# Optimization experiments

Hardware: AMD Instinct MI355X
Metric: run time of the kernel (lower is better)

The kernel has to match this reference:

```python
import jax, jax.numpy as jnp
import numpy as np

B, S, H = 32, 64, 512
ATT = 128


def _window_index_tables(seq_len):
    # Enumerate all contiguous windows of size 2..S, same set (order-independent
    # for the softmax-weighted sum) as the torch double loop.
    starts, ends = [], []
    for w in range(2, seq_len + 1):
        for s in range(0, seq_len - w + 1):
            starts.append(s)
            ends.append(s + w)
    starts = np.asarray(starts, np.int32)
    ends = np.asarray(ends, np.int32)
    widths = ends - starts
    ks = np.floor(np.log2(widths)).astype(np.int32)  # sparse-table level per window
    e2 = ends - (1 << ks)                            # second gather position
    return starts, e2, ks


def setup_inputs() -> dict:
    key = jax.random.key(0)
    k0, k1, k2, k3, k4 = jax.random.split(key, 5)
    return {
        "lstm_out": jax.random.normal(k0, (B, S, H), dtype=jnp.float32),
        "W1": jax.random.normal(k1, (H, ATT), dtype=jnp.float32) * 0.05,
        "b1": jax.random.normal(k2, (ATT,), dtype=jnp.float32) * 0.05,
        "W2": jax.random.normal(k3, (ATT, 1), dtype=jnp.float32) * 0.05,
        "b2": jax.random.normal(k4, (1,), dtype=jnp.float32) * 0.05,
    }


def reference(lstm_out, W1, b1, W2, b2):
    b, s, h = lstm_out.shape
    # Sparse table: M[k][:, i] = max over lstm_out[:, i : i+2^k] (clipped to s).
    n_levels = int(np.floor(np.log2(s))) + 1
    tables = [lstm_out]
    for k in range(1, n_levels):
        half = 1 << (k - 1)
        prev = tables[-1]
        shifted = jnp.concatenate(
            [prev[:, half:], jnp.full((b, half, h), -jnp.inf, prev.dtype)], axis=1)
        tables.append(jnp.maximum(prev, shifted))
    Mstack = jnp.stack(tables)  # [K, B, S, H]

    starts, e2, ks = _window_index_tables(s)
    # Range max of each window = max of two overlapping power-of-two blocks.
    pooled = jnp.maximum(Mstack[ks, :, starts], Mstack[ks, :, e2])  # [n_win, B, H]
    pooled = jnp.transpose(pooled, (1, 0, 2))  # [B, n_win, H]

    hid = jax.nn.relu(jnp.einsum("bnh,ha->bna", pooled, W1) + b1)
    scores = jnp.einsum("bna,ao->bno", hid, W2) + b2  # [B, n_win, 1]
    attn = jax.nn.softmax(scores, axis=1)
    return jnp.sum(attn * pooled, axis=1)  # [B, H]
```

## Files before the change

### kernel.cpp

```cpp
#include <hip/hip_runtime.h>
#include <stdint.h>

typedef unsigned short u16;
typedef unsigned int u32;

#define B_    32
#define S_    64
#define H_    512
#define ATT_  128
#define NWIN  2016
#define NLEV  7

typedef __bf16 bf16x8 __attribute__((ext_vector_type(8)));
typedef float  f32x4  __attribute__((ext_vector_type(4)));

__device__ __forceinline__ float bf2f(u16 u) {
  union { u32 i; float f; } v; v.i = ((u32)u) << 16; return v.f;
}
__device__ __forceinline__ u16 f2bf(float f) {
  union { float f; u32 i; } v; v.f = f;
  u32 i = v.i;
  i += 0x7fffu + ((i >> 16) & 1u);
  return (u16)(i >> 16);
}
__device__ __forceinline__ u32 bfmax2(u32 a, u32 b) {
  u16 a0 = (u16)(a & 0xffffu), a1 = (u16)(a >> 16);
  u16 b0 = (u16)(b & 0xffffu), b1 = (u16)(b >> 16);
  u16 m0 = (bf2f(a0) >= bf2f(b0)) ? a0 : b0;
  u16 m1 = (bf2f(a1) >= bf2f(b1)) ? a1 : b1;
  return (u32)m0 | ((u32)m1 << 16);
}
__device__ __forceinline__ uint4 bfmax8(uint4 a, uint4 b) {
  uint4 m;
  m.x = bfmax2(a.x, b.x); m.y = bfmax2(a.y, b.y);
  m.z = bfmax2(a.z, b.z); m.w = bfmax2(a.w, b.w);
  return m;
}

__launch_bounds__(256)
__global__ void k0_init(const float* __restrict__ W1, u16* __restrict__ w1t,
                        u16* __restrict__ widx) {
  int tid = threadIdx.x;
  if (blockIdx.x == 0) {
    for (int n = tid; n < NWIN; n += 256) {
      int w = 2, rem = n;
      while (rem >= 65 - w) { rem -= 65 - w; ++w; }
      int s = rem;
      int k = 31 - __clz(w);
      int e2 = s + w - (1 << k);
      widx[n] = (u16)(s | (e2 << 6) | (k << 12));
    }
  }
  int gid = blockIdx.x * 256 + tid;
  for (int idx = gid; idx < H_ * ATT_; idx += 64 * 256) {
    int n = idx >> 9, kq = idx & 511;
    w1t[idx] = f2bf(W1[kq * ATT_ + n]);
  }
}

__launch_bounds__(256)
__global__ void k1_table(const float* __restrict__ lstm, u16* __restrict__ table) {
  int hc = blockIdx.x, b = blockIdx.y, tid = threadIdx.x;
  __shared__ u16 bufA[64 * 64], bufB[64 * 64];
  const float* src = lstm + (size_t)b * S_ * H_ + hc * 64;
  u16* tb = table + (size_t)b * NLEV * S_ * H_ + hc * 64;
  for (int t = tid; t < 64 * 16; t += 256) {
    int r = t >> 4, c4 = t & 15;
    float4 f = *reinterpret_cast<const float4*>(src + r * H_ + c4 * 4);
    ushort4 u;
    u.x = f2bf(f.x); u.y = f2bf(f.y); u.z = f2bf(f.z); u.w = f2bf(f.w);
    *reinterpret_cast<ushort4*>(&bufA[r * 64 + c4 * 4]) = u;
    *reinterpret_cast<ushort4*>(tb + r * H_ + c4 * 4) = u;
  }
  u16* pa = bufA; u16* pb = bufB;
  for (int k = 1; k < NLEV; ++k) {
    __syncthreads();
    int half = 1 << (k - 1);
    u16* dst_g = tb + k * S_ * H_;
    for (int t = tid; t < 64 * 16; t += 256) {
      int r = t >> 4, c4 = t & 15;
      int r2 = r + half; if (r2 > 63) r2 = 63;
      uint2 a  = *reinterpret_cast<const uint2*>(&pa[r  * 64 + c4 * 4]);
      uint2 bq = *reinterpret_cast<const uint2*>(&pa[r2 * 64 + c4 * 4]);
      uint2 m; m.x = bfmax2(a.x, bq.x); m.y = bfmax2(a.y, bq.y);
      *reinterpret_cast<uint2*>(&pb[r * 64 + c4 * 4]) = m;
      *reinterpret_cast<uint2*>(dst_g + r * H_ + c4 * 4) = m;
    }
    u16* tmp = pa; pa = pb; pb = tmp;
  }
}

__launch_bounds__(256)
__global__ void k2_scores(const u16* __restrict__ table, const u16* __restrict__ w1t,
                          const float* __restrict__ b1, const float* __restrict__ w2,
                          const u16* __restrict__ widx, float* __restrict__ scores) {
  const int b = blockIdx.y, mt = blockIdx.x;
  __shared__ u16 As[96 * 72];
  __shared__ u16 Bs[128 * 72];
  __shared__ u16 widx_l[96];
  __shared__ float b1s[128], w2s[128], sc[96];
  int tid = threadIdx.x;
  if (tid < 96) { widx_l[tid] = widx[mt * 96 + tid]; sc[tid] = 0.f; }
  if (tid < 128) { b1s[tid] = b1[tid]; w2s[tid] = w2[tid]; }
  __syncthreads();

  const u16* tb = table + (size_t)b * NLEV * S_ * H_;
  int wid = tid >> 6, lane = tid & 63;
  int wm = wid & 1, wn = wid >> 1;
  int lrow = lane & 15, quad = lane >> 4;

  f32x4 acc[3][4];
#pragma unroll
  for (int i = 0; i < 3; ++i)
#pragma unroll
    for (int j = 0; j < 4; ++j) acc[i][j] = (f32x4){0.f, 0.f, 0.f, 0.f};

  for (int kk = 0; kk < H_; kk += 64) {
    for (int t = tid; t < 768; t += 256) {
      int r = t >> 3, c = t & 7;
      int pk = widx_l[r];
      int s = pk & 63, e2 = (pk >> 6) & 63, lv = pk >> 12;
      uint4 va = *reinterpret_cast<const uint4*>(tb + (lv * S_ + s) * H_ + kk + c * 8);
      uint4 vb = *reinterpret_cast<const uint4*>(tb + (lv * S_ + e2) * H_ + kk + c * 8);
      uint4 vm = bfmax8(va, vb);
      *reinterpret_cast<uint4*>(&As[r * 72 + c * 8]) = vm;
    }
    for (int t = tid; t < 1024; t += 256) {
      int n = t >> 3, c = t & 7;
      uint4 v = *reinterpret_cast<const uint4*>(w1t + n * H_ + kk + c * 8);
      *reinterpret_cast<uint4*>(&Bs[n * 72 + c * 8]) = v;
    }
    __syncthreads();
#pragma unroll
    for (int ks = 0; ks < 64; ks += 32) {
      bf16x8 af[3], bfr[4];
#pragma unroll
      for (int i = 0; i < 3; ++i)
        af[i] = *reinterpret_cast<const bf16x8*>(&As[(wm * 48 + i * 16 + lrow) * 72 + ks + quad * 8]);
#pragma unroll
      for (int j = 0; j < 4; ++j)
        bfr[j] = *reinterpret_cast<const bf16x8*>(&Bs[(wn * 64 + j * 16 + lrow) * 72 + ks + quad * 8]);
#pragma unroll
      for (int i = 0; i < 3; ++i)
#pragma unroll
        for (int j = 0; j < 4; ++j)
          acc[i][j] = __builtin_amdgcn_mfma_f32_16x16x32_bf16(af[i], bfr[j], acc[i][j], 0, 0, 0);
    }
    __syncthreads();
  }

#pragma unroll
  for (int i = 0; i < 3; ++i) {
#pragma unroll
    for (int r = 0; r < 4; ++r) {
      float p = 0.f;
#pragma unroll
      for (int j = 0; j < 4; ++j) {
        int n = wn * 64 + j * 16 + lrow;
        float v = acc[i][j][r] + b1s[n];
        p += (v > 0.f ? v : 0.f) * w2s[n];
      }
      p += __shfl_xor(p, 1, 16);
      p += __shfl_xor(p, 2, 16);
      p += __shfl_xor(p, 4, 16);
      p += __shfl_xor(p, 8, 16);
      if (lrow == 0) atomicAdd(&sc[wm * 48 + i * 16 + quad * 4 + r], p);
    }
  }
  __syncthreads();
  if (tid < 96) scores[b * NWIN + mt * 96 + tid] = sc[tid];
}

__launch_bounds__(256)
__global__ void k3_softmax(const float* __restrict__ scores, float* __restrict__ attn) {
  int b = blockIdx.x, tid = threadIdx.x;
  __shared__ float red[256];
  float mx = -1e30f;
  for (int n = tid; n < NWIN; n += 256) mx = fmaxf(mx, scores[b * NWIN + n]);
  red[tid] = mx; __syncthreads();
  for (int s = 128; s > 0; s >>= 1) {
    if (tid < s) red[tid] = fmaxf(red[tid], red[tid + s]);
    __syncthreads();
  }
  mx = red[0]; __syncthreads();
  float sum = 0.f;
  for (int n = tid; n < NWIN; n += 256) {
    float e = __expf(scores[b * NWIN + n] - mx);
    attn[b * NWIN + n] = e;
    sum += e;
  }
  red[tid] = sum; __syncthreads();
  for (int s = 128; s > 0; s >>= 1) {
    if (tid < s) red[tid] += red[tid + s];
    __syncthreads();
  }
  float inv = 1.f / red[0];
  __syncthreads();
  for (int n = tid; n < NWIN; n += 256) attn[b * NWIN + n] *= inv;
}

__launch_bounds__(256)
__global__ void k4_out(const u16* __restrict__ table, const float* __restrict__ attn,
                       const u16* __restrict__ widx, float* __restrict__ out) {
  int hc = blockIdx.x, b = blockIdx.y, tid = threadIdx.x;
  __shared__ u16 Tl[6 * 64 * 32];
  __shared__ float attn_l[NWIN];
  __shared__ u16 widx_l[NWIN];
  __shared__ float red[8][32];
  const u16* tb = table + (size_t)b * NLEV * S_ * H_ + S_ * H_;
  int h0 = hc * 32;
  for (int t = tid; t < 6 * 64 * 4; t += 256) {
    int row = t >> 2, c = t & 3;
    uint4 v = *reinterpret_cast<const uint4*>(tb + row * H_ + h0 + c * 8);
    *reinterpret_cast<uint4*>(&Tl[row * 32 + c * 8]) = v;
  }
  for (int n = tid; n < NWIN; n += 256) {
    attn_l[n] = attn[b * NWIN + n];
    widx_l[n] = widx[n];
  }
  __syncthreads();
  int h = tid & 31, g = tid >> 5;
  float acc = 0.f;
  for (int n = g * 252; n < g * 252 + 252; ++n) {
    int pk = widx_l[n];
    int s = pk & 63, e2 = (pk >> 6) & 63, lv = pk >> 12;
    float va = bf2f(Tl[((lv - 1) * 64 + s) * 32 + h]);
    float vb = bf2f(Tl[((lv - 1) * 64 + e2) * 32 + h]);
    acc += attn_l[n] * fmaxf(va, vb);
  }
  red[g][h] = acc;
  __syncthreads();
  if (tid < 32) {
    float sum = 0.f;
#pragma unroll
    for (int g2 = 0; g2 < 8; ++g2) sum += red[g2][tid];
    out[b * H_ + h0 + tid] = sum;
  }
}

extern "C" void kernel_launch(void* const* d_in, const int* in_sizes, int n_in,
                              void* d_out, int out_size, void* d_ws, size_t ws_size,
                              hipStream_t stream) {
  const float* lstm = (const float*)d_in[0];
  const float* W1   = (const float*)d_in[1];
  const float* b1   = (const float*)d_in[2];
  const float* W2   = (const float*)d_in[3];
  float* out = (float*)d_out;

  char* ws = (char*)d_ws;
  u16*   widx   = (u16*)(ws + 0);
  u16*   w1t    = (u16*)(ws + 4096);
  u16*   table  = (u16*)(ws + 135168);
  float* scores = (float*)(ws + 14815232);
  float* attn   = (float*)(ws + 15073280);

  k0_init   <<<64, 256, 0, stream>>>(W1, w1t, widx);
  k1_table  <<<dim3(8, B_), 256, 0, stream>>>(lstm, table);
  k2_scores <<<dim3(21, B_), 256, 0, stream>>>(table, w1t, b1, W2, widx, scores);
  k3_softmax<<<B_, 256, 0, stream>>>(scores, attn);
  k4_out    <<<dim3(16, B_), 256, 0, stream>>>(table, attn, widx, out);
}
```

Measured before the change: 133.6 us.

## Fuse init/table and softmax/output kernels, register-prefetch GEMM tiles in scores kernel

Merges the W1-transpose/window-index kernel with the sparse-table build into one launch. It also folds the softmax into the output kernel, which reduces via wave shuffles and applies the normalization at the end. The scores GEMM now prefetches the next K-chunk of gathered table rows and W1 into registers while MFMAs run on the current LDS tile, and it sets an occupancy hint of 3 blocks. bfmax2 now uses float fmaxf on shifted bits. The aim is to cut two launches and the intermediate attn buffer, and to hide global-load latency in the GEMM, at the cost of higher register pressure and redundant softmax work in each of the 16 h-chunk blocks.

Result: no change. 133.2 us (-0.3%).

```diff
diff --git a/kernel.cpp b/kernel.cpp
--- a/kernel.cpp
+++ b/kernel.cpp
@@ -14,21 +14,23 @@
 typedef __bf16 bf16x8 __attribute__((ext_vector_type(8)));
 typedef float  f32x4  __attribute__((ext_vector_type(4)));
 
-__device__ __forceinline__ float bf2f(u16 u) {
-  union { u32 i; float f; } v; v.i = ((u32)u) << 16; return v.f;
-}
+__device__ __forceinline__ float asf(u32 i) {
+  union { u32 i; float f; } v; v.i = i; return v.f;
+}
+__device__ __forceinline__ u32 asu(float f) {
+  union { float f; u32 i; } v; v.f = f; return v.i;
+}
+__device__ __forceinline__ float bf2f(u16 u) { return asf(((u32)u) << 16); }
 __device__ __forceinline__ u16 f2bf(float f) {
-  union { float f; u32 i; } v; v.f = f;
-  u32 i = v.i;
+  u32 i = asu(f);
   i += 0x7fffu + ((i >> 16) & 1u);
   return (u16)(i >> 16);
 }
 __device__ __forceinline__ u32 bfmax2(u32 a, u32 b) {
-  u16 a0 = (u16)(a & 0xffffu), a1 = (u16)(a >> 16);
-  u16 b0 = (u16)(b & 0xffffu), b1 = (u16)(b >> 16);
-  u16 m0 = (bf2f(a0) >= bf2f(b0)) ? a0 : b0;
-  u16 m1 = (bf2f(a1) >= bf2f(b1)) ? a1 : b1;
-  return (u32)m0 | ((u32)m1 << 16);
+  float a0 = asf(a << 16), a1 = asf(a & 0xffff0000u);
+  float b0 = asf(b << 16), b1 = asf(b & 0xffff0000u);
+  u32 m0 = asu(fmaxf(a0, b0)), m1 = asu(fmaxf(a1, b1));
+  return (m1 & 0xffff0000u) | (m0 >> 16);
 }
 __device__ __forceinline__ uint4 bfmax8(uint4 a, uint4 b) {
   uint4 m;
@@ -38,59 +40,60 @@
 }
 
 __launch_bounds__(256)
-__global__ void k0_init(const float* __restrict__ W1, u16* __restrict__ w1t,
-                        u16* __restrict__ widx) {
-  int tid = threadIdx.x;
-  if (blockIdx.x == 0) {
-    for (int n = tid; n < NWIN; n += 256) {
-      int w = 2, rem = n;
-      while (rem >= 65 - w) { rem -= 65 - w; ++w; }
-      int s = rem;
-      int k = 31 - __clz(w);
-      int e2 = s + w - (1 << k);
-      widx[n] = (u16)(s | (e2 << 6) | (k << 12));
-    }
-  }
-  int gid = blockIdx.x * 256 + tid;
-  for (int idx = gid; idx < H_ * ATT_; idx += 64 * 256) {
-    int n = idx >> 9, kq = idx & 511;
-    w1t[idx] = f2bf(W1[kq * ATT_ + n]);
-  }
-}
-
-__launch_bounds__(256)
-__global__ void k1_table(const float* __restrict__ lstm, u16* __restrict__ table) {
-  int hc = blockIdx.x, b = blockIdx.y, tid = threadIdx.x;
+__global__ void k01_init(const float* __restrict__ lstm, const float* __restrict__ W1,
+                         u16* __restrict__ table, u16* __restrict__ w1t,
+                         u16* __restrict__ widx) {
+  int bid = blockIdx.x, tid = threadIdx.x;
   __shared__ u16 bufA[64 * 64], bufB[64 * 64];
-  const float* src = lstm + (size_t)b * S_ * H_ + hc * 64;
-  u16* tb = table + (size_t)b * NLEV * S_ * H_ + hc * 64;
-  for (int t = tid; t < 64 * 16; t += 256) {
-    int r = t >> 4, c4 = t & 15;
-    float4 f = *reinterpret_cast<const float4*>(src + r * H_ + c4 * 4);
-    ushort4 u;
-    u.x = f2bf(f.x); u.y = f2bf(f.y); u.z = f2bf(f.z); u.w = f2bf(f.w);
-    *reinterpret_cast<ushort4*>(&bufA[r * 64 + c4 * 4]) = u;
-    *reinterpret_cast<ushort4*>(tb + r * H_ + c4 * 4) = u;
-  }
-  u16* pa = bufA; u16* pb = bufB;
-  for (int k = 1; k < NLEV; ++k) {
-    __syncthreads();
-    int half = 1 << (k - 1);
-    u16* dst_g = tb + k * S_ * H_;
+  if (bid < 256) {
+    int hc = bid & 7, b = bid >> 3;
+    const float* src = lstm + (size_t)b * S_ * H_ + hc * 64;
+    u16* tb = table + (size_t)b * NLEV * S_ * H_ + hc * 64;
     for (int t = tid; t < 64 * 16; t += 256) {
       int r = t >> 4, c4 = t & 15;
-      int r2 = r + half; if (r2 > 63) r2 = 63;
-      uint2 a  = *reinterpret_cast<const uint2*>(&pa[r  * 64 + c4 * 4]);
-      uint2 bq = *reinterpret_cast<const uint2*>(&pa[r2 * 64 + c4 * 4]);
-      uint2 m; m.x = bfmax2(a.x, bq.x); m.y = bfmax2(a.y, bq.y);
-      *reinterpret_cast<uint2*>(&pb[r * 64 + c4 * 4]) = m;
-      *reinterpret_cast<uint2*>(dst_g + r * H_ + c4 * 4) = m;
-    }
-    u16* tmp = pa; pa = pb; pb = tmp;
-  }
-}
-
-__launch_bounds__(256)
+      float4 f = *reinterpret_cast<const float4*>(src + r * H_ + c4 * 4);
+      ushort4 u;
+      u.x = f2bf(f.x); u.y = f2bf(f.y); u.z = f2bf(f.z); u.w = f2bf(f.w);
+      *reinterpret_cast<ushort4*>(&bufA[r * 64 + c4 * 4]) = u;
+      *reinterpret_cast<ushort4*>(tb + r * H_ + c4 * 4) = u;
+    }
+    u16* pa = bufA; u16* pb = bufB;
+    for (int k = 1; k < NLEV; ++k) {
+      __syncthreads();
+      int half = 1 << (k - 1);
+      u16* dst_g = tb + k * S_ * H_;
+      for (int t = tid; t < 64 * 16; t += 256) {
+        int r = t >> 4, c4 = t & 15;
+        int r2 = r + half; if (r2 > 63) r2 = 63;
+        uint2 a  = *reinterpret_cast<const uint2*>(&pa[r  * 64 + c4 * 4]);
+        uint2 bq = *reinterpret_cast<const uint2*>(&pa[r2 * 64 + c4 * 4]);
+        uint2 m; m.x = bfmax2(a.x, bq.x); m.y = bfmax2(a.y, bq.y);
+        *reinterpret_cast<uint2*>(&pb[r * 64 + c4 * 4]) = m;
+        *reinterpret_cast<uint2*>(dst_g + r * H_ + c4 * 4) = m;
+      }
+      u16* tmp = pa; pa = pb; pb = tmp;
+    }
+  } else {
+    int gb = bid - 256;
+    if (gb == 0) {
+      for (int n = tid; n < NWIN; n += 256) {
+        int w = 2, rem = n;
+        while (rem >= 65 - w) { rem -= 65 - w; ++w; }
+        int s = rem;
+        int k = 31 - __clz(w);
+        int e2 = s + w - (1 << k);
+        widx[n] = (u16)(s | (e2 << 6) | (k << 12));
+      }
+    }
+    for (int q = tid; q < 2048; q += 256) {
+      int idx = gb * 2048 + q;
+      int n = idx >> 9, kq = idx & 511;
+      w1t[idx] = f2bf(W1[kq * ATT_ + n]);
+    }
+  }
+}
+
+__launch_bounds__(256, 3)
 __global__ void k2_scores(const u16* __restrict__ table, const u16* __restrict__ w1t,
                           const float* __restrict__ b1, const float* __restrict__ w2,
                           const u16* __restrict__ widx, float* __restrict__ scores) {
@@ -105,6 +108,33 @@
   __syncthreads();
 
   const u16* tb = table + (size_t)b * NLEV * S_ * H_;
+  int ar[3], ac[3];
+  const u16 *apa[3], *apb[3];
+#pragma unroll
+  for (int i = 0; i < 3; ++i) {
+    int t = tid + i * 256; ar[i] = t >> 3; ac[i] = t & 7;
+    int pk = widx_l[ar[i]];
+    int s = pk & 63, e2 = (pk >> 6) & 63, lv = pk >> 12;
+    apa[i] = tb + (lv * S_ + s) * H_ + ac[i] * 8;
+    apb[i] = tb + (lv * S_ + e2) * H_ + ac[i] * 8;
+  }
+  int bn[4], bc[4];
+#pragma unroll
+  for (int j = 0; j < 4; ++j) {
+    int t = tid + j * 256; bn[j] = t >> 3; bc[j] = t & 7;
+  }
+
+  uint4 ra[3], rb[3], rB[4];
+#define ISSUE(KK) do { \
+  _Pragma("unroll") for (int i = 0; i < 3; ++i) { \
+    ra[i] = *reinterpret_cast<const uint4*>(apa[i] + (KK)); \
+    rb[i] = *reinterpret_cast<const uint4*>(apb[i] + (KK)); } \
+  _Pragma("unroll") for (int j = 0; j < 4; ++j) \
+    rB[j] = *reinterpret_cast<const uint4*>(w1t + bn[j] * H_ + (KK) + bc[j] * 8); \
+} while (0)
+
+  ISSUE(0);
+
   int wid = tid >> 6, lane = tid & 63;
   int wm = wid & 1, wn = wid >> 1;
   int lrow = lane & 15, quad = lane >> 4;
@@ -115,22 +145,19 @@
 #pragma unroll
     for (int j = 0; j < 4; ++j) acc[i][j] = (f32x4){0.f, 0.f, 0.f, 0.f};
 
-  for (int kk = 0; kk < H_; kk += 64) {
-    for (int t = tid; t < 768; t += 256) {
-      int r = t >> 3, c = t & 7;
-      int pk = widx_l[r];
-      int s = pk & 63, e2 = (pk >> 6) & 63, lv = pk >> 12;
-      uint4 va = *reinterpret_cast<const uint4*>(tb + (lv * S_ + s) * H_ + kk + c * 8);
-      uint4 vb = *reinterpret_cast<const uint4*>(tb + (lv * S_ + e2) * H_ + kk + c * 8);
-      uint4 vm = bfmax8(va, vb);
-      *reinterpret_cast<uint4*>(&As[r * 72 + c * 8]) = vm;
-    }
-    for (int t = tid; t < 1024; t += 256) {
-      int n = t >> 3, c = t & 7;
-      uint4 v = *reinterpret_cast<const uint4*>(w1t + n * H_ + kk + c * 8);
-      *reinterpret_cast<uint4*>(&Bs[n * 72 + c * 8]) = v;
-    }
+  for (int kc = 0; kc < 8; ++kc) {
+    uint4 mA[3];
+#pragma unroll
+    for (int i = 0; i < 3; ++i) mA[i] = bfmax8(ra[i], rb[i]);
     __syncthreads();
+#pragma unroll
+    for (int i = 0; i < 3; ++i)
+      *reinterpret_cast<uint4*>(&As[ar[i] * 72 + ac[i] * 8]) = mA[i];
+#pragma unroll
+    for (int j = 0; j < 4; ++j)
+      *reinterpret_cast<uint4*>(&Bs[bn[j] * 72 + bc[j] * 8]) = rB[j];
+    __syncthreads();
+    if (kc < 7) ISSUE((kc + 1) * 64);
 #pragma unroll
     for (int ks = 0; ks < 64; ks += 32) {
       bf16x8 af[3], bfr[4];
@@ -146,8 +173,8 @@
         for (int j = 0; j < 4; ++j)
           acc[i][j] = __builtin_amdgcn_mfma_f32_16x16x32_bf16(af[i], bfr[j], acc[i][j], 0, 0, 0);
     }
-    __syncthreads();
-  }
+  }
+#undef ISSUE
 
 #pragma unroll
   for (int i = 0; i < 3; ++i) {
@@ -172,53 +199,48 @@
 }
 
 __launch_bounds__(256)
-__global__ void k3_softmax(const float* __restrict__ scores, float* __restrict__ attn) {
-  int b = blockIdx.x, tid = threadIdx.x;
-  __shared__ float red[256];
-  float mx = -1e30f;
-  for (int n = tid; n < NWIN; n += 256) mx = fmaxf(mx, scores[b * NWIN + n]);
-  red[tid] = mx; __syncthreads();
-  for (int s = 128; s > 0; s >>= 1) {
-    if (tid < s) red[tid] = fmaxf(red[tid], red[tid + s]);
-    __syncthreads();
-  }
-  mx = red[0]; __syncthreads();
-  float sum = 0.f;
-  for (int n = tid; n < NWIN; n += 256) {
-    float e = __expf(scores[b * NWIN + n] - mx);
-    attn[b * NWIN + n] = e;
-    sum += e;
-  }
-  red[tid] = sum; __syncthreads();
-  for (int s = 128; s > 0; s >>= 1) {
-    if (tid < s) red[tid] += red[tid + s];
-    __syncthreads();
-  }
-  float inv = 1.f / red[0];
-  __syncthreads();
-  for (int n = tid; n < NWIN; n += 256) attn[b * NWIN + n] *= inv;
-}
-
-__launch_bounds__(256)
-__global__ void k4_out(const u16* __restrict__ table, const float* __restrict__ attn,
-                       const u16* __restrict__ widx, float* __restrict__ out) {
+__global__ void k34_out(const u16* __restrict__ table, const float* __restrict__ scores,
+                        const u16* __restrict__ widx, float* __restrict__ out) {
   int hc = blockIdx.x, b = blockIdx.y, tid = threadIdx.x;
   __shared__ u16 Tl[6 * 64 * 32];
   __shared__ float attn_l[NWIN];
   __shared__ u16 widx_l[NWIN];
   __shared__ float red[8][32];
+  __shared__ float wredM[4], wredS[4];
   const u16* tb = table + (size_t)b * NLEV * S_ * H_ + S_ * H_;
   int h0 = hc * 32;
+  int lane = tid & 63, wid = tid >> 6;
+
   for (int t = tid; t < 6 * 64 * 4; t += 256) {
     int row = t >> 2, c = t & 3;
     uint4 v = *reinterpret_cast<const uint4*>(tb + row * H_ + h0 + c * 8);
     *reinterpret_cast<uint4*>(&Tl[row * 32 + c * 8]) = v;
   }
+  for (int n = tid; n < NWIN; n += 256) widx_l[n] = widx[n];
+
+  float mx = -1e30f;
   for (int n = tid; n < NWIN; n += 256) {
-    attn_l[n] = attn[b * NWIN + n];
-    widx_l[n] = widx[n];
-  }
-  __syncthreads();
+    float v = scores[b * NWIN + n];
+    attn_l[n] = v;
+    mx = fmaxf(mx, v);
+  }
+#pragma unroll
+  for (int off = 32; off > 0; off >>= 1) mx = fmaxf(mx, __shfl_xor(mx, off, 64));
+  if (lane == 0) wredM[wid] = mx;
+  __syncthreads();
+  mx = fmaxf(fmaxf(wredM[0], wredM[1]), fmaxf(wredM[2], wredM[3]));
+  float sum = 0.f;
+  for (int n = tid; n < NWIN; n += 256) {
+    float e = __expf(attn_l[n] - mx);
+    attn_l[n] = e;
+    sum += e;
+  }
+#pragma unroll
+  for (int off = 32; off > 0; off >>= 1) sum += __shfl_xor(sum, off, 64);
+  if (lane == 0) wredS[wid] = sum;
+  __syncthreads();
+  float inv = 1.f / (wredS[0] + wredS[1] + wredS[2] + wredS[3]);
+
   int h = tid & 31, g = tid >> 5;
   float acc = 0.f;
   for (int n = g * 252; n < g * 252 + 252; ++n) {
@@ -231,10 +253,10 @@
   red[g][h] = acc;
   __syncthreads();
   if (tid < 32) {
-    float sum = 0.f;
-#pragma unroll
-    for (int g2 = 0; g2 < 8; ++g2) sum += red[g2][tid];
-    out[b * H_ + h0 + tid] = sum;
+    float s2 = 0.f;
+#pragma unroll
+    for (int g2 = 0; g2 < 8; ++g2) s2 += red[g2][tid];
+    out[b * H_ + h0 + tid] = s2 * inv;
   }
 }
 
@@ -252,11 +274,8 @@
   u16*   w1t    = (u16*)(ws + 4096);
   u16*   table  = (u16*)(ws + 135168);
   float* scores = (float*)(ws + 14815232);
-  float* attn   = (float*)(ws + 15073280);
-
-  k0_init   <<<64, 256, 0, stream>>>(W1, w1t, widx);
-  k1_table  <<<dim3(8, B_), 256, 0, stream>>>(lstm, table);
-  k2_scores <<<dim3(21, B_), 256, 0, stream>>>(table, w1t, b1, W2, widx, scores);
-  k3_softmax<<<B_, 256, 0, stream>>>(scores, attn);
-  k4_out    <<<dim3(16, B_), 256, 0, stream>>>(table, attn, widx, out);
-}
+
+  k01_init <<<288, 256, 0, stream>>>(lstm, W1, table, w1t, widx);
+  k2_scores<<<dim3(21, B_), 256, 0, stream>>>(table, w1t, b1, W2, widx, scores);
+  k34_out  <<<dim3(16, B_), 256, 0, stream>>>(table, scores, widx, out);
+}
```
